# Performance work log

Hardware: AMD Instinct MI355X
Metric: run time of the kernel (lower is better)

## Reference

```python
import jax, jax.numpy as jnp
import numpy as np

D_MODEL = 768; N_HEADS = 24; HEAD_DIM = 64; D_INNER = 1536
D_STATE = 128; CONV_K = 4
CONV_DIM = D_INNER + 2 * D_STATE              # 1792
PROJ_DIM = 2 * D_INNER + 2 * D_STATE + N_HEADS  # 3352
CHUNK = 256; N_LAYERS = 24; EPS = 1e-5


def rms(h, w):
    return h * jax.lax.rsqrt(jnp.mean(h * h, -1, keepdims=True) + EPS) * w


def bnorm(x, g, b, m, v):
    shp = (1, -1) + (1,) * (x.ndim - 2)
    return (x - m.reshape(shp)) * (g.reshape(shp) / jnp.sqrt(v.reshape(shp) + EPS)) + b.reshape(shp)


def conv1d(x, w, b, stride, pad, groups=1):
    y = jax.lax.conv_general_dilated(x, w, (stride,), [pad], feature_group_count=groups,
                                     dimension_numbers=('NCH', 'OIH', 'NCH'))
    return y + b[None, :, None]


def ssd(X, dA, Bm, Cm, chunk):
    # X:(b,l,h,p) already multiplied by dt; dA:(b,l,h)=dt*A (negative); Bm,Cm:(b,l,h,n)
    b, l, h, p = X.shape
    n = Bm.shape[-1]
    c = l // chunk
    Xc = X.reshape(b, c, chunk, h, p)
    Bc = Bm.reshape(b, c, chunk, h, n)
    Cc = Cm.reshape(b, c, chunk, h, n)
    Ac = dA.reshape(b, c, chunk, h).transpose(0, 3, 1, 2)   # (b,h,c,k)
    Acs = jnp.cumsum(Ac, axis=-1)
    seg = Acs[..., :, None] - Acs[..., None, :]              # (b,h,c,k,k)
    tri = jnp.tril(jnp.ones((chunk, chunk), bool))
    Lm = jnp.where(tri, jnp.exp(seg), 0.0)
    Y_diag = jnp.einsum('bckhn,bcshn,bhcks,bcshp->bckhp', Cc, Bc, Lm, Xc)
    decay_states = jnp.exp(Acs[..., -1:] - Acs)              # (b,h,c,k)
    states = jnp.einsum('bckhn,bhck,bckhp->bchpn', Bc, decay_states, Xc)
    chunk_decay = jnp.exp(Acs[..., -1])                      # (b,h,c)
    def step(carry, inp):
        st, dec = inp
        return carry * dec[..., None, None] + st, carry
    _, prev = jax.lax.scan(step, jnp.zeros_like(states[:, 0]),
                           (states.transpose(1, 0, 2, 3, 4), chunk_decay.transpose(2, 0, 1)))
    prev = prev.transpose(1, 0, 2, 3, 4)                     # (b,c,h,p,n)
    Y_off = jnp.einsum('bckhn,bchpn,bhck->bckhp', Cc, prev, jnp.exp(Acs))
    return (Y_diag + Y_off).reshape(b, l, h, p)


def forward(x, c1_w, c1_b, bn1_g, bn1_b, bn1_m, bn1_v, c2_w, c2_b, bn2_g, bn2_b, bn2_m, bn2_v,
            c3_w, c3_b, bn3_g, bn3_b, bn3_m, bn3_v, ln_w, in_proj_w, conv_w, conv_b, dt_bias,
            A_log, D_skip, gn_w, out_proj_w, normf_w, fc1_w, fc1_b, bnc_g, bnc_b, bnc_m, bnc_v,
            fc2_w, fc2_b):
    gelu = lambda t: jax.nn.gelu(t, approximate=False)
    h = bnorm(gelu(conv1d(x, c1_w, c1_b, 2, (2, 2))), bn1_g, bn1_b, bn1_m, bn1_v)
    h = bnorm(gelu(conv1d(h, c2_w, c2_b, 2, (1, 1))), bn2_g, bn2_b, bn2_m, bn2_v)
    h = bnorm(gelu(conv1d(h, c3_w, c3_b, 1, (1, 1))), bn3_g, bn3_b, bn3_m, bn3_v)
    h = h.transpose(0, 2, 1)  # (B, L, D)

    def layer(h, p):
        lnw, inw, cw, cb, dtb, alog, dsk, gnw, outw = p
        b, l, _ = h.shape
        zxbcdt = rms(h, lnw) @ inw                  # (B,L,3352)
        z = zxbcdt[..., :D_INNER]
        xBC = zxbcdt[..., D_INNER:D_INNER + CONV_DIM]
        dt = jax.nn.softplus(zxbcdt[..., D_INNER + CONV_DIM:] + dtb)  # (B,L,H)
        xBC = jax.nn.silu(conv1d(xBC.transpose(0, 2, 1), cw[:, None, :], cb, 1,
                                 (CONV_K - 1, 0), groups=CONV_DIM)).transpose(0, 2, 1)
        Xh = xBC[..., :D_INNER].reshape(b, l, N_HEADS, HEAD_DIM)
        Bh = jnp.broadcast_to(xBC[..., D_INNER:D_INNER + D_STATE][:, :, None, :],
                              (b, l, N_HEADS, D_STATE))
        Ch = jnp.broadcast_to(xBC[..., D_INNER + D_STATE:][:, :, None, :],
                              (b, l, N_HEADS, D_STATE))
        dA = dt * (-jnp.exp(alog))[None, None, :]
        Y = ssd(Xh * dt[..., None], dA, Bh, Ch, CHUNK) + dsk[None, None, :, None] * Xh
        y = rms(Y.reshape(b, l, D_INNER) * jax.nn.silu(z), gnw)  # gated RMSNorm
        return h + y @ outw, None

    h, _ = jax.lax.scan(jax.checkpoint(layer), h,
                        (ln_w, in_proj_w, conv_w, conv_b, dt_bias, A_log, D_skip, gn_w, out_proj_w))
    pooled = rms(h, normf_w).mean(1)
    f = jax.nn.relu(bnorm(pooled @ fc1_w + fc1_b, bnc_g, bnc_b, bnc_m, bnc_v))
    return f @ fc2_w + fc2_b


def setup_inputs() -> dict:
    key = jax.random.key(0)
    it = iter(jax.random.split(key, 40))
    nx = lambda shp, s: jax.random.normal(next(it), shp, jnp.float32) * s
    B, L0 = 2, 4096
    inp = {}
    inp['x'] = nx((B, 12, L0), 1.0)
    inp['c1_w'] = nx((192, 12, 5), 0.1); inp['c1_b'] = jnp.zeros(192)
    inp['bn1_g'] = jnp.ones(192); inp['bn1_b'] = jnp.zeros(192)
    inp['bn1_m'] = jnp.zeros(192); inp['bn1_v'] = jnp.ones(192)
    inp['c2_w'] = nx((384, 192, 3), 0.05); inp['c2_b'] = jnp.zeros(384)
    inp['bn2_g'] = jnp.ones(384); inp['bn2_b'] = jnp.zeros(384)
    inp['bn2_m'] = jnp.zeros(384); inp['bn2_v'] = jnp.ones(384)
    inp['c3_w'] = nx((768, 384, 3), 0.05); inp['c3_b'] = jnp.zeros(768)
    inp['bn3_g'] = jnp.ones(768); inp['bn3_b'] = jnp.zeros(768)
    inp['bn3_m'] = jnp.zeros(768); inp['bn3_v'] = jnp.ones(768)
    inp['ln_w'] = jnp.ones((N_LAYERS, D_MODEL))
    inp['in_proj_w'] = nx((N_LAYERS, D_MODEL, PROJ_DIM), 0.02)
    inp['conv_w'] = nx((N_LAYERS, CONV_DIM, CONV_K), 0.2)
    inp['conv_b'] = jnp.zeros((N_LAYERS, CONV_DIM))
    inp['dt_bias'] = nx((N_LAYERS, N_HEADS), 0.5)
    inp['A_log'] = jnp.log(jnp.tile(jnp.arange(1, N_HEADS + 1, dtype=jnp.float32)[None], (N_LAYERS, 1)))
    inp['D_skip'] = jnp.ones((N_LAYERS, N_HEADS))
    inp['gn_w'] = jnp.ones((N_LAYERS, D_INNER))
    inp['out_proj_w'] = nx((N_LAYERS, D_INNER, D_MODEL), 0.02)
    inp['normf_w'] = jnp.ones(D_MODEL)
    inp['fc1_w'] = nx((D_MODEL, 512), 0.05); inp['fc1_b'] = jnp.zeros(512)
    inp['bnc_g'] = jnp.ones(512); inp['bnc_b'] = jnp.zeros(512)
    inp['bnc_m'] = jnp.zeros(512); inp['bnc_v'] = jnp.ones(512)
    inp['fc2_w'] = nx((512, 27), 0.05); inp['fc2_b'] = jnp.zeros(27)
    return inp


def reference(x, c1_w, c1_b, bn1_g, bn1_b, bn1_m, bn1_v, c2_w, c2_b, bn2_g, bn2_b, bn2_m, bn2_v,
              c3_w, c3_b, bn3_g, bn3_b, bn3_m, bn3_v, ln_w, in_proj_w, conv_w, conv_b, dt_bias,
              A_log, D_skip, gn_w, out_proj_w, normf_w, fc1_w, fc1_b, bnc_g, bnc_b, bnc_m, bnc_v,
              fc2_w, fc2_b):
    return forward(x, c1_w, c1_b, bn1_g, bn1_b, bn1_m, bn1_v, c2_w, c2_b, bn2_g, bn2_b, bn2_m,
                   bn2_v, c3_w, c3_b, bn3_g, bn3_b, bn3_m, bn3_v, ln_w, in_proj_w, conv_w,
                   conv_b, dt_bias, A_log, D_skip, gn_w, out_proj_w, normf_w, fc1_w, fc1_b,
                   bnc_g, bnc_b, bnc_m, bnc_v, fc2_w, fc2_b)
```

## Files before the change

kernel.cpp:

```cpp
#include <hip/hip_runtime.h>
#include <math.h>

#define DEV __device__ __forceinline__

constexpr int BATCH = 2;
constexpr int L0 = 4096;
constexpr int LS1 = 2048;
constexpr int LS2 = 1024;
constexpr int SEQ = 1024;
constexpr int DM = 768;
constexpr int NH = 24;
constexpr int HD = 64;
constexpr int DI = 1536;
constexpr int DSTATE = 128;
constexpr int CDIM = 1792;
constexpr int PDIM = 3352;
constexpr int PPAD = 3456;
constexpr int CHUNKC = 256;
constexpr int NCH = 4;
constexpr int NLAYER = 24;
constexpr float EPSF = 1e-5f;

constexpr int XT2_ROWS = 2050;
constexpr size_t XT2_BSTRIDE = (size_t)XT2_ROWS*192;
constexpr int XT3_ROWS = 1026;
constexpr size_t XT3_BSTRIDE = (size_t)XT3_ROWS*384;

typedef short bf16x8 __attribute__((ext_vector_type(8)));
typedef float f32x4 __attribute__((ext_vector_type(4)));

DEV float sigmoidf_(float x){ return 1.f/(1.f+expf(-x)); }
DEV float siluf_(float x){ return x*sigmoidf_(x); }
DEV float geluf_(float x){ return 0.5f*x*(1.f+erff(x*0.70710678118654752440f)); }
DEV float softplusf_(float x){ return fmaxf(x,0.f) + log1pf(expf(-fabsf(x))); }

DEV unsigned short f2bf(float x){
  union { float f; unsigned int u; } v; v.f = x;
  unsigned int u = v.u;
  unsigned int r = (u + 0x7fffu + ((u>>16)&1u)) >> 16;
  return (unsigned short)r;
}
DEV float bf2f(unsigned short u){
  union { unsigned int u; float f; } v; v.u = ((unsigned int)u)<<16; return v.f;
}

DEV void load_lds16(const void* g, void* l){
  __builtin_amdgcn_global_load_lds(
      (const __attribute__((address_space(1))) unsigned int*)g,
      (__attribute__((address_space(3))) unsigned int*)l,
      16, 0, 0);
}

DEV float block_sum_256(float v, float* red4){
  #pragma unroll
  for (int o=32;o>0;o>>=1) v += __shfl_down(v,o,64);
  int tid = threadIdx.x;
  __syncthreads();
  if ((tid&63)==0) red4[tid>>6]=v;
  __syncthreads();
  return red4[0]+red4[1]+red4[2]+red4[3];
}

__global__ __launch_bounds__(256) void conv_stem1(const float* __restrict__ x,
    const float* __restrict__ w, const float* __restrict__ bias,
    const float* __restrict__ g, const float* __restrict__ bb,
    const float* __restrict__ mn, const float* __restrict__ vr,
    float* __restrict__ out){
  int idx = blockIdx.x*256+threadIdx.x;
  if (idx >= BATCH*192*LS1) return;
  int lo = idx & (LS1-1);
  int co = (idx >> 11) % 192;
  int b  = idx / (192*LS1);
  float s = bias[co];
  const float* wr = w + co*60;
  #pragma unroll
  for (int ci=0; ci<12; ci++){
    const float* xr = x + ((size_t)(b*12+ci))*L0;
    #pragma unroll
    for (int k=0;k<5;k++){
      int li = lo*2 + k - 2;
      if (li>=0 && li<L0) s += wr[ci*5+k]*xr[li];
    }
  }
  s = geluf_(s);
  s = (s-mn[co])*(g[co]*rsqrtf(vr[co]+EPSF)) + bb[co];
  out[idx] = s;
}

__global__ __launch_bounds__(256) void wt_reorder(const float* __restrict__ w,
    unsigned short* __restrict__ o, int CO, int CI, int KK){
  int idx = blockIdx.x*256+threadIdx.x;
  if (idx >= CO*CI*KK) return;
  int ci = idx % CI;
  int k  = (idx/CI) % KK;
  int co = idx/(CI*KK);
  o[idx] = f2bf(w[(size_t)co*CI*KK + (size_t)ci*KK + k]);
}

__global__ __launch_bounds__(256) void transpose_pad_bf(const float* __restrict__ in,
    unsigned short* __restrict__ out, int R, int C,
    size_t in_bstride, size_t out_bstride){
  const float* ib = in + (size_t)blockIdx.z*in_bstride;
  unsigned short* ob = out + (size_t)blockIdx.z*out_bstride;
  __shared__ float t[32][33];
  int c0 = blockIdx.x*32, r0 = blockIdx.y*32;
  int tx = threadIdx.x & 31, ty = threadIdx.x >> 5;
  #pragma unroll
  for (int i=0;i<32;i+=8)
    t[ty+i][tx] = ib[(size_t)(r0+ty+i)*C + c0+tx];
  __syncthreads();
  #pragma unroll
  for (int i=0;i<32;i+=8)
    ob[(size_t)(c0+ty+i+1)*R + r0+tx] = f2bf(t[tx][ty+i]);
  if (blockIdx.x==0 && ty==0){
    ob[r0+tx] = 0;
    ob[(size_t)(C+1)*R + r0+tx] = 0;
  }
}

__global__ __launch_bounds__(256) void zero_rows3(unsigned short* __restrict__ xT3){
  int i = blockIdx.x*256+threadIdx.x;
  if (i >= 2*2*384) return;
  int ci = i % 384;
  int r  = (i/384) & 1;
  int b2 = i / 768;
  xT3[(size_t)b2*XT3_BSTRIDE + (size_t)(r?1025:0)*384 + ci] = 0;
}

template<int MODE>
__global__ __launch_bounds__(256,2) void gemm_stem(const unsigned short* __restrict__ A,
    const unsigned short* __restrict__ Bt,
    const float* __restrict__ bias, const float* __restrict__ g,
    const float* __restrict__ bbn, const float* __restrict__ mn,
    const float* __restrict__ vr,
    unsigned short* __restrict__ Ob, float* __restrict__ Of,
    int K, int rowStride, size_t batchStride){
  __shared__ alignas(16) unsigned short As[2][128*32];
  __shared__ alignas(16) unsigned short Bs[2][128*32];
  int tid = threadIdx.x;
  int wave = tid >> 6, lane = tid & 63;
  int mBase = blockIdx.y*128, nBase = blockIdx.x*128;
  int bidx = mBase >> 10;
  int mloc = mBase & 1023;
  const unsigned short* Ab = A + (size_t)bidx*batchStride + (size_t)mloc*rowStride;
  const size_t rs2 = (size_t)rowStride*2;
  const size_t K2 = (size_t)K*2;
  int o0 = wave*1024 + lane*16;
  int o1 = o0 + 4096;
  const char* Ag0 = (const char*)Ab + (size_t)(o0>>6)*rs2 + (o0&63);
  const char* Ag1 = (const char*)Ab + (size_t)(o1>>6)*rs2 + (o1&63);
  const char* Bg0 = (const char*)Bt + (size_t)(nBase + (o0>>6))*K2 + (o0&63);
  const char* Bg1 = (const char*)Bt + (size_t)(nBase + (o1>>6))*K2 + (o1&63);

  int wm = (wave>>1)*64, wn = (wave&1)*64;
  int ln = lane & 15, quad = lane >> 4;

  f32x4 acc[4][4];
  #pragma unroll
  for (int i=0;i<4;i++)
    #pragma unroll
    for (int j=0;j<4;j++) acc[i][j] = (f32x4){0.f,0.f,0.f,0.f};

  auto stage = [&](int buf, int k0){
    size_t kb = (size_t)k0*2;
    char* AsW = (char*)(&As[buf][0]) + wave*1024;
    char* BsW = (char*)(&Bs[buf][0]) + wave*1024;
    load_lds16(Ag0 + kb, AsW);
    load_lds16(Ag1 + kb, AsW + 4096);
    load_lds16(Bg0 + kb, BsW);
    load_lds16(Bg1 + kb, BsW + 4096);
  };

  stage(0, 0);
  int cur = 0;
  for (int k0=0; k0<K; k0+=32){
    __syncthreads();
    if (k0+32 < K) stage(cur^1, k0+32);
    bf16x8 a[4], b[4];
    #pragma unroll
    for (int mt=0;mt<4;mt++)
      a[mt] = *(const bf16x8*)((const char*)(&As[cur][0]) + (size_t)(wm+mt*16+ln)*64 + quad*16);
    #pragma unroll
    for (int nt=0;nt<4;nt++)
      b[nt] = *(const bf16x8*)((const char*)(&Bs[cur][0]) + (size_t)(wn+nt*16+ln)*64 + quad*16);
    #pragma unroll
    for (int mt=0;mt<4;mt++)
      #pragma unroll
      for (int nt=0;nt<4;nt++)
        acc[mt][nt] = __builtin_amdgcn_mfma_f32_16x16x32_bf16(a[mt], b[nt], acc[mt][nt], 0,0,0);
    cur ^= 1;
  }

  #pragma unroll
  for (int nt=0;nt<4;nt++){
    int col = nBase + wn + nt*16 + ln;
    float bs = bias[col];
    float sc = g[col]*rsqrtf(vr[col]+EPSF);
    float bnm2 = mn[col], bnb2 = bbn[col];
    #pragma unroll
    for (int mt=0;mt<4;mt++){
      int row0 = mBase + wm + mt*16 + quad*4;
      #pragma unroll
      for (int r=0;r<4;r++){
        int row = row0 + r;
        float v = acc[mt][nt][r] + bs;
        v = geluf_(v);
        v = (v-bnm2)*sc + bnb2;
        if (MODE==0){
          int b2 = row >> 10, lr = row & 1023;
          Ob[(size_t)b2*XT3_BSTRIDE + (size_t)(lr+1)*384 + col] = f2bf(v);
        } else {
          Of[(size_t)row*DM + col] = v;
        }
      }
    }
  }
}

template<int BF>
__global__ __launch_bounds__(256) void rmsnorm768(const float* __restrict__ in,
    const float* __restrict__ w, float* __restrict__ outf, unsigned short* __restrict__ outb){
  int row = blockIdx.x;
  const float* p = in + (size_t)row*DM;
  float v0[3]; float ss=0.f;
  #pragma unroll
  for (int t=0;t<3;t++){ float q = p[threadIdx.x + t*256]; v0[t]=q; ss+=q*q; }
  __shared__ float red[4];
  float tot = block_sum_256(ss, red);
  float sc = rsqrtf(tot*(1.f/DM) + EPSF);
  #pragma unroll
  for (int t=0;t<3;t++){
    int d = threadIdx.x + t*256;
    float o = v0[t]*sc*w[d];
    if (BF) outb[(size_t)row*DM + d] = f2bf(o);
    else    outf[(size_t)row*DM + d] = o;
  }
}

__global__ __launch_bounds__(256) void transpose_cvt_l(const float* __restrict__ in0,
    unsigned short* __restrict__ out0, int R, int Cin, int Cpad,
    size_t in_lstride, size_t out_lstride,
    const float* __restrict__ rsc, size_t rsc_stride){
  const float* in = in0 + (size_t)blockIdx.z*in_lstride;
  unsigned short* out = out0 + (size_t)blockIdx.z*out_lstride;
  const float* rs = rsc ? (rsc + (size_t)blockIdx.z*rsc_stride) : nullptr;
  __shared__ float t[32][33];
  int c0 = blockIdx.x*32, r0 = blockIdx.y*32;
  int tx = threadIdx.x & 31, ty = threadIdx.x >> 5;
  #pragma unroll
  for (int i=0;i<32;i+=8){
    int r = r0+ty+i, c = c0+tx;
    float v = (c<Cin) ? in[(size_t)r*Cin + c] : 0.f;
    if (rs) v *= rs[r];
    t[ty+i][tx] = v;
  }
  __syncthreads();
  #pragma unroll
  for (int i=0;i<32;i+=8){
    int c = c0+ty+i, r = r0+tx;
    if (c < Cpad) out[(size_t)c*R + r] = f2bf(t[tx][ty+i]);
  }
}

template<int MODE>
__global__ __launch_bounds__(256,2) void gemm_bf16(const unsigned short* __restrict__ A,
    const unsigned short* __restrict__ Bt, float* __restrict__ Cf,
    unsigned short* __restrict__ Cb, int Ntrue, int K, int ldc){
  __shared__ alignas(16) unsigned short As[2][128*32];
  __shared__ alignas(16) unsigned short Bs[2][128*32];
  int tid = threadIdx.x;
  int wave = tid >> 6, lane = tid & 63;
  int mBase = blockIdx.y*128, nBase = blockIdx.x*128;
  const size_t K2 = (size_t)K*2;
  int o0 = wave*1024 + lane*16;
  int o1 = o0 + 4096;
  const char* Ag0 = (const char*)A + (size_t)(mBase + (o0>>6))*K2 + (o0&63);
  const char* Ag1 = (const char*)A + (size_t)(mBase + (o1>>6))*K2 + (o1&63);
  const char* Bg0 = (const char*)Bt + (size_t)(nBase + (o0>>6))*K2 + (o0&63);
  const char* Bg1 = (const char*)Bt + (size_t)(nBase + (o1>>6))*K2 + (o1&63);

  int wm = (wave>>1)*64, wn = (wave&1)*64;
  int ln = lane & 15, quad = lane >> 4;

  f32x4 acc[4][4];
  #pragma unroll
  for (int i=0;i<4;i++)
    #pragma unroll
    for (int j=0;j<4;j++) acc[i][j] = (f32x4){0.f,0.f,0.f,0.f};

  auto stage = [&](int buf, int k0){
    size_t kb = (size_t)k0*2;
    char* AsW = (char*)(&As[buf][0]) + wave*1024;
    char* BsW = (char*)(&Bs[buf][0]) + wave*1024;
    load_lds16(Ag0 + kb, AsW);
    load_lds16(Ag1 + kb, AsW + 4096);
    load_lds16(Bg0 + kb, BsW);
    load_lds16(Bg1 + kb, BsW + 4096);
  };

  stage(0, 0);
  int cur = 0;
  for (int k0=0; k0<K; k0+=32){
    __syncthreads();
    if (k0+32 < K) stage(cur^1, k0+32);
    bf16x8 a[4], b[4];
    #pragma unroll
    for (int mt=0;mt<4;mt++)
      a[mt] = *(const bf16x8*)((const char*)(&As[cur][0]) + (size_t)(wm+mt*16+ln)*64 + quad*16);
    #pragma unroll
    for (int nt=0;nt<4;nt++)
      b[nt] = *(const bf16x8*)((const char*)(&Bs[cur][0]) + (size_t)(wn+nt*16+ln)*64 + quad*16);
    #pragma unroll
    for (int mt=0;mt<4;mt++)
      #pragma unroll
      for (int nt=0;nt<4;nt++)
        acc[mt][nt] = __builtin_amdgcn_mfma_f32_16x16x32_bf16(a[mt], b[nt], acc[mt][nt], 0,0,0);
    cur ^= 1;
  }

  #pragma unroll
  for (int mt=0;mt<4;mt++){
    #pragma unroll
    for (int nt=0;nt<4;nt++){
      int col = nBase + wn + nt*16 + ln;
      int row0 = mBase + wm + mt*16 + quad*4;
      if (col < Ntrue){
        #pragma unroll
        for (int r=0;r<4;r++){
          float v = acc[mt][nt][r];
          if (MODE==2) Cb[(size_t)(row0+r)*ldc + col] = f2bf(v);
          else         Cf[(size_t)(row0+r)*ldc + col] = v;
        }
      }
    }
  }
}

__global__ __launch_bounds__(256,2) void gemm_out(const unsigned short* __restrict__ A,
    const unsigned short* __restrict__ Bt, const float* __restrict__ ssum,
    float* __restrict__ C, int N, int K){
  __shared__ alignas(16) unsigned short As[2][64*136];
  __shared__ alignas(16) unsigned short Bs[2][64*136];
  int tid = threadIdx.x;
  int wave = tid>>6, lane = tid&63, ln = lane&15, quad = lane>>4;
  int mBase = blockIdx.y*64, nBase = blockIdx.x*64;
  int srow = tid>>2, sseg = tid&3;
  const unsigned short* Ag = A + (size_t)(mBase+srow)*K;
  const unsigned short* Bg = Bt + (size_t)(nBase+srow)*K;

  bf16x8 rA[4], rB[4];
  auto ldregs = [&](int k0){
    #pragma unroll
    for (int s=0;s<4;s++){
      rA[s] = *(const bf16x8*)(Ag + k0 + (sseg+s*4)*8);
      rB[s] = *(const bf16x8*)(Bg + k0 + (sseg+s*4)*8);
    }
  };
  auto stlds = [&](int buf){
    #pragma unroll
    for (int s=0;s<4;s++){
      *(bf16x8*)&As[buf][srow*136 + (sseg+s*4)*8] = rA[s];
      *(bf16x8*)&Bs[buf][srow*136 + (sseg+s*4)*8] = rB[s];
    }
  };

  f32x4 acc[4];
  #pragma unroll
  for (int nt=0;nt<4;nt++) acc[nt] = (f32x4){0.f,0.f,0.f,0.f};

  ldregs(0); stlds(0);
  int cur = 0;
  for (int k0=0; k0<K; k0+=128){
    __syncthreads();
    bool pf = (k0+128 < K);
    if (pf) ldregs(k0+128);
    bf16x8 a[4];
    #pragma unroll
    for (int kq=0;kq<4;kq++)
      a[kq] = *(const bf16x8*)&As[cur][(wave*16+ln)*136 + kq*32 + quad*8];
    #pragma unroll
    for (int nt=0;nt<4;nt++){
      #pragma unroll
      for (int kq=0;kq<4;kq++){
        bf16x8 b = *(const bf16x8*)&Bs[cur][(nt*16+ln)*136 + kq*32 + quad*8];
        acc[nt] = __builtin_amdgcn_mfma_f32_16x16x32_bf16(a[kq], b, acc[nt], 0,0,0);
      }
    }
    if (pf) stlds(cur^1);
    cur ^= 1;
  }
  int row0 = mBase + wave*16 + quad*4;
  #pragma unroll
  for (int r=0;r<4;r++){
    int row = row0 + r;
    float rsv = rsqrtf(ssum[row]*(1.f/DI) + EPSF);
    #pragma unroll
    for (int nt=0;nt<4;nt++){
      int col = nBase + nt*16 + ln;
      float* p = C + (size_t)row*N + col;
      *p += acc[nt][r]*rsv;
    }
  }
}

__global__ __launch_bounds__(256) void dwconv8(const unsigned short* __restrict__ zxb,
    const float* __restrict__ w, const float* __restrict__ bias,
    unsigned short* __restrict__ out, float* __restrict__ ssum){
  int idx = blockIdx.x*256+threadIdx.x;
  if (idx < BATCH*SEQ) ssum[idx] = 0.f;
  if (idx >= BATCH*SEQ*(CDIM/8)) return;
  int c8 = idx % (CDIM/8);
  int l  = (idx/(CDIM/8)) % SEQ;
  int b  = idx / ((CDIM/8)*SEQ);
  int c = c8*8;
  float acc[8];
  #pragma unroll
  for (int j=0;j<8;j++) acc[j] = bias[c+j];
  const unsigned short* colbase = zxb + (size_t)(b*SEQ)*PDIM + DI + c;
  #pragma unroll
  for (int k=0;k<4;k++){
    int li = l-3+k;
    if (li>=0){
      bf16x8 v = *(const bf16x8*)(colbase + (size_t)li*PDIM);
      #pragma unroll
      for (int j=0;j<8;j++) acc[j] += w[(c+j)*4+k]*bf2f((unsigned short)v[j]);
    }
  }
  unsigned short o[8];
  #pragma unroll
  for (int j=0;j<8;j++) o[j] = f2bf(siluf_(acc[j]));
  *(bf16x8*)(out + (size_t)idx*8) = *(bf16x8*)&o[0];
}

__global__ __launch_bounds__(256) void prep_fused(const unsigned short* __restrict__ zxb,
    const unsigned short* __restrict__ xbcb,
    const float* __restrict__ dtb, const float* __restrict__ alog,
    float* __restrict__ acs, unsigned short* __restrict__ XdT,
    unsigned short* __restrict__ Xdec, unsigned short* __restrict__ BTg){
  int blk = blockIdx.x;
  int tid = threadIdx.x;
  __shared__ alignas(16) unsigned short Xs[64*72];
  __shared__ float dts[256];
  __shared__ float dec[256];
  __shared__ float wsum[4];
  if (blk < 192){
    int c = blk % NCH, h = (blk/NCH) % NH, b = blk/(NCH*NH);
    int bh = b*NH + h;
    int l = c*CHUNKC + tid;
    int lane = tid & 63, wv = tid >> 6;
    float negA = -expf(alog[h]);
    float lg = bf2f(zxb[((size_t)(b*SEQ+l))*PDIM + (DI+CDIM) + h]) + dtb[h];
    float dt = softplusf_(lg);
    dts[tid] = dt;
    float s = dt*negA;
    #pragma unroll
    for (int off=1; off<64; off<<=1){
      float t = __shfl_up(s, off, 64);
      if (lane >= off) s += t;
    }
    if (lane == 63) wsum[wv] = s;
    __syncthreads();
    float pre = 0.f, tot = 0.f;
    #pragma unroll
    for (int w=0; w<4; w++){
      float wv2 = wsum[w];
      if (w < wv) pre += wv2;
      tot += wv2;
    }
    s += pre;
    acs[(size_t)bh*SEQ + l] = s;
    dec[tid] = expf(tot - s);
    int srow = tid>>2, sseg = tid&3;
    int p = tid>>2, lq = tid&3;
    for (int lt2=0; lt2<4; lt2++){
      int lt = c*4 + lt2;
      __syncthreads();
      const unsigned short* src = xbcb + ((size_t)(b*SEQ) + lt*64 + srow)*CDIM + h*HD;
      #pragma unroll
      for (int s2=0;s2<2;s2++)
        *(bf16x8*)&Xs[srow*72 + (sseg+s2*4)*8] = *(const bf16x8*)(src + (sseg+s2*4)*8);
      __syncthreads();
      unsigned short o1[16], o2[16];
      #pragma unroll
      for (int li=0; li<16; li++){
        int j = lq*16+li;
        int lc = lt2*64 + j;
        float vv = bf2f(Xs[j*72 + p]) * dts[lc];
        o1[li] = f2bf(vv);
        o2[li] = f2bf(vv*dec[lc]);
      }
      size_t rowo = ((size_t)bh*HD + p)*SEQ + lt*64 + lq*16;
      *(bf16x8*)(XdT + rowo)     = *(bf16x8*)&o1[0];
      *(bf16x8*)(XdT + rowo + 8) = *(bf16x8*)&o1[8];
      *(bf16x8*)(Xdec + rowo)     = *(bf16x8*)&o2[0];
      *(bf16x8*)(Xdec + rowo + 8) = *(bf16x8*)&o2[8];
    }
  } else {
    int r = blk - 192;
    int nh = r & 1, lt = (r>>1) & 15, b = r >> 5;
    int srow = tid>>2, sseg = tid&3;
    const unsigned short* src = xbcb + ((size_t)(b*SEQ) + lt*64 + srow)*CDIM + DI + nh*64;
    #pragma unroll
    for (int s2=0;s2<2;s2++)
      *(bf16x8*)&Xs[srow*72 + (sseg+s2*4)*8] = *(const bf16x8*)(src + (sseg+s2*4)*8);
    __syncthreads();
    int n = tid>>2, lq = tid&3;
    unsigned short o[16];
    #pragma unroll
    for (int li=0; li<16; li++) o[li] = Xs[(lq*16+li)*72 + n];
    size_t rowo = ((size_t)b*DSTATE + nh*64 + n)*SEQ + lt*64 + lq*16;
    *(bf16x8*)(BTg + rowo)     = *(bf16x8*)&o[0];
    *(bf16x8*)(BTg + rowo + 8) = *(bf16x8*)&o[8];
  }
}

__global__ __launch_bounds__(256) void ssd_states2(const unsigned short* __restrict__ Xdec,
    const unsigned short* __restrict__ BTg, float* __restrict__ states){
  int blk = blockIdx.x;
  int nh = blk & 1;
  int r = blk >> 1;
  int h = r % NH;  r /= NH;
  int c = r % NCH;
  int b = r / NCH;
  int tid = threadIdx.x, wave = tid>>6, lane = tid&63, ln = lane&15, quad = lane>>4;
  __shared__ alignas(16) unsigned short As[64*264];
  __shared__ alignas(16) unsigned short Bs[64*264];
  int bh = b*NH + h;
  {
    int srow = tid>>2, sseg = tid&3;
    const unsigned short* ga = Xdec + ((size_t)bh*HD + srow)*SEQ + c*CHUNKC;
    const unsigned short* gb = BTg + ((size_t)b*DSTATE + nh*64 + srow)*SEQ + c*CHUNKC;
    #pragma unroll
    for (int s=0;s<8;s++){
      *(bf16x8*)&As[srow*264 + (sseg+s*4)*8] = *(const bf16x8*)(ga + (sseg+s*4)*8);
      *(bf16x8*)&Bs[srow*264 + (sseg+s*4)*8] = *(const bf16x8*)(gb + (sseg+s*4)*8);
    }
  }
  __syncthreads();
  f32x4 acc[4];
  #pragma unroll
  for (int nt=0;nt<4;nt++) acc[nt] = (f32x4){0.f,0.f,0.f,0.f};
  bf16x8 a[8];
  #pragma unroll
  for (int kq=0;kq<8;kq++)
    a[kq] = *(const bf16x8*)&As[(wave*16+ln)*264 + kq*32 + quad*8];
  #pragma unroll
  for (int nt=0;nt<4;nt++){
    #pragma unroll
    for (int kq=0;kq<8;kq++){
      bf16x8 bb = *(const bf16x8*)&Bs[(nt*16+ln)*264 + kq*32 + quad*8];
      acc[nt] = __builtin_amdgcn_mfma_f32_16x16x32_bf16(a[kq], bb, acc[nt], 0,0,0);
    }
  }
  float* sp = states + (((size_t)(b*NCH+c)*NH + h) << 13) + nh*64;
  #pragma unroll
  for (int nt=0;nt<4;nt++){
    #pragma unroll
    for (int r2=0;r2<4;r2++)
      sp[(size_t)(wave*16 + quad*4 + r2)*DSTATE + nt*16 + ln] = acc[nt][r2];
  }
}

__global__ __launch_bounds__(256) void ssd_scan(const float* __restrict__ states,
    const float* __restrict__ acs, unsigned short* __restrict__ prev){
  int idx = blockIdx.x*256+threadIdx.x;
  if (idx >= BATCH*NH*HD*DSTATE) return;
  int pn = idx & 8191;
  int bh = idx >> 13;
  int h = bh % NH, b = bh / NH;
  float carry = 0.f;
  #pragma unroll
  for (int c=0;c<NCH;c++){
    size_t o = (((size_t)(b*NCH+c)*NH + h) << 13) + pn;
    prev[o] = f2bf(carry);
    float dec = expf(acs[(b*NH+h)*SEQ + c*CHUNKC + CHUNKC-1]);
    carry = carry*dec + states[o];
  }
}

constexpr int CW_S  = 136;
constexpr int SB_S  = 72;
constexpr int XT_S  = 72;

__global__ __launch_bounds__(256,2) void ssd_diag2(
    const unsigned short* __restrict__ xbcb, const unsigned short* __restrict__ XdT,
    const float* __restrict__ acs, const unsigned short* __restrict__ prev,
    const float* __restrict__ dskip, const unsigned short* __restrict__ zxb,
    float* __restrict__ ssum, unsigned short* __restrict__ Y){
  int blk = blockIdx.x;
  int t = blk & 3;
  int r0 = blk >> 2;
  int h = r0 % NH;  r0 /= NH;
  int c = r0 % NCH;
  int b = r0 / NCH;

  int tid = threadIdx.x;
  int wave = tid>>6, lane = tid&63, ln = lane&15, quad = lane>>4;

  __shared__ float ac[CHUNKC];
  __shared__ alignas(16) unsigned short Cw[64*CW_S];
  __shared__ alignas(16) unsigned short Pv[64*CW_S];
  __shared__ alignas(16) unsigned short Bt[64*CW_S];
  __shared__ alignas(16) unsigned short Xt[64*XT_S];
  __shared__ alignas(16) unsigned short Sb[4][16*SB_S];

  const int bh = b*NH + h;
  const size_t rowbase = (size_t)(b*SEQ + c*CHUNKC);

  ac[tid] = acs[(size_t)bh*SEQ + c*CHUNKC + tid];

  {
    int srow = tid>>2, sseg = tid&3;
    const unsigned short* gc = xbcb + (rowbase + t*64 + srow)*CDIM + DI + DSTATE;
    const unsigned short* gp = prev + (((size_t)(b*NCH+c)*NH + h) << 13) + (size_t)srow*DSTATE;
    #pragma unroll
    for (int s=0;s<4;s++){
      *(bf16x8*)&Cw[srow*CW_S + (sseg+s*4)*8] = *(const bf16x8*)(gc + (sseg+s*4)*8);
      *(bf16x8*)&Pv[srow*CW_S + (sseg+s*4)*8] = *(const bf16x8*)(gp + (sseg+s*4)*8);
    }
  }
  __syncthreads();

  bf16x8 aC[4];
  #pragma unroll
  for (int kq=0;kq<4;kq++)
    aC[kq] = *(const bf16x8*)&Cw[(wave*16+ln)*CW_S + kq*32 + quad*8];

  f32x4 yacc[4];
  #pragma unroll
  for (int ps=0;ps<4;ps++) yacc[ps] = (f32x4){0.f,0.f,0.f,0.f};

  for (int jt=0; jt<=t; jt++){
    __syncthreads();
    {
      int srow = tid>>2, sseg = tid&3;
      const unsigned short* gbm = xbcb + (rowbase + jt*64 + srow)*CDIM + DI;
      #pragma unroll
      for (int s=0;s<4;s++)
        *(bf16x8*)&Bt[srow*CW_S + (sseg+s*4)*8] = *(const bf16x8*)(gbm + (sseg+s*4)*8);
      const unsigned short* gx = XdT + ((size_t)bh*HD + srow)*SEQ + c*CHUNKC + jt*64;
      #pragma unroll
      for (int s=0;s<2;s++)
        *(bf16x8*)&Xt[srow*XT_S + (sseg+s*4)*8] = *(const bf16x8*)(gx + (sseg+s*4)*8);
    }
    __syncthreads();

    #pragma unroll
    for (int js=0; js<4; js++){
      f32x4 s = (f32x4){0.f,0.f,0.f,0.f};
      #pragma unroll
      for (int kq=0;kq<4;kq++){
        bf16x8 bB = *(const bf16x8*)&Bt[(js*16+ln)*CW_S + kq*32 + quad*8];
        s = __builtin_amdgcn_mfma_f32_16x16x32_bf16(aC[kq], bB, s, 0,0,0);
      }
      int jc = jt*64 + js*16 + ln;
      #pragma unroll
      for (int r=0;r<4;r++){
        int icl = t*64 + wave*16 + quad*4 + r;
        float d = (jc<=icl) ? (ac[icl]-ac[jc]) : -1e30f;
        Sb[wave][(quad*4+r)*SB_S + js*16 + ln] = f2bf(expf(d)*s[r]);
      }
    }
    bf16x8 aS[2];
    #pragma unroll
    for (int kq=0;kq<2;kq++)
      aS[kq] = *(const bf16x8*)&Sb[wave][ln*SB_S + kq*32 + quad*8];
    #pragma unroll
    for (int ps=0;ps<4;ps++){
      #pragma unroll
      for (int kq=0;kq<2;kq++){
        bf16x8 bX = *(const bf16x8*)&Xt[(ps*16+ln)*XT_S + kq*32 + quad*8];
        yacc[ps] = __builtin_amdgcn_mfma_f32_16x16x32_bf16(aS[kq], bX, yacc[ps], 0,0,0);
      }
    }
  }

  f32x4 oacc[4];
  #pragma unroll
  for (int ps=0;ps<4;ps++) oacc[ps] = (f32x4){0.f,0.f,0.f,0.f};
  #pragma unroll
  for (int ps=0;ps<4;ps++){
    #pragma unroll
    for (int kq=0;kq<4;kq++){
      bf16x8 bP = *(const bf16x8*)&Pv[(ps*16+ln)*CW_S + kq*32 + quad*8];
      oacc[ps] = __builtin_amdgcn_mfma_f32_16x16x32_bf16(aC[kq], bP, oacc[ps], 0,0,0);
    }
  }

  float dsk = dskip[h];
  #pragma unroll
  for (int r=0;r<4;r++){
    int icl = t*64 + wave*16 + quad*4 + r;
    float ei = expf(ac[icl]);
    size_t l = rowbase + icl;
    float rss = 0.f;
    #pragma unroll
    for (int ps=0;ps<4;ps++){
      int p = ps*16 + ln;
      float xraw = bf2f(xbcb[l*CDIM + h*HD + p]);
      float zv = bf2f(zxb[l*PDIM + h*HD + p]);
      float yg = (yacc[ps][r] + ei*oacc[ps][r] + dsk*xraw) * siluf_(zv);
      Y[l*DI + h*HD + p] = f2bf(yg);
      rss += yg*yg;
    }
    rss += __shfl_down(rss, 8, 64);
    rss += __shfl_down(rss, 4, 64);
    rss += __shfl_down(rss, 2, 64);
    rss += __shfl_down(rss, 1, 64);
    if (ln == 0) atomicAdd(&ssum[l], rss);
  }
}

__global__ __launch_bounds__(256) void mean_pool(const float* __restrict__ hn,
    float* __restrict__ pooled){
  int idx = blockIdx.x*256+threadIdx.x;
  if (idx >= BATCH*DM) return;
  int b = idx / DM, d = idx % DM;
  float s = 0.f;
  for (int l=0;l<SEQ;l++) s += hn[((size_t)(b*SEQ+l))*DM + d];
  pooled[idx] = s * (1.f/SEQ);
}

__global__ __launch_bounds__(512) void head_k(const float* __restrict__ pooled,
    const float* __restrict__ w1, const float* __restrict__ b1,
    const float* __restrict__ g, const float* __restrict__ bb,
    const float* __restrict__ mn, const float* __restrict__ vr,
    const float* __restrict__ w2, const float* __restrict__ b2,
    float* __restrict__ out){
  int b = blockIdx.x;
  int j = threadIdx.x;
  __shared__ float f[512];
  __shared__ float pl[DM];
  for (int t=j; t<DM; t+=512) pl[t] = pooled[b*DM+t];
  __syncthreads();
  float s = b1[j];
  for (int k=0;k<DM;k++) s += pl[k]*w1[k*512+j];
  s = (s-mn[j])*(g[j]*rsqrtf(vr[j]+EPSF)) + bb[j];
  f[j] = fmaxf(s,0.f);
  __syncthreads();
  if (j < 27){
    float o = b2[j];
    for (int k=0;k<512;k++) o += f[k]*w2[k*27+j];
    out[b*27+j] = o;
  }
}

extern "C" void kernel_launch(void* const* d_in, const int* in_sizes, int n_in,
                              void* d_out, int out_size, void* d_ws, size_t ws_size,
                              hipStream_t stream){
  const float* x      = (const float*)d_in[0];
  const float* c1_w   = (const float*)d_in[1];
  const float* c1_b   = (const float*)d_in[2];
  const float* bn1_g  = (const float*)d_in[3];
  const float* bn1_b  = (const float*)d_in[4];
  const float* bn1_m  = (const float*)d_in[5];
  const float* bn1_v  = (const float*)d_in[6];
  const float* c2_w   = (const float*)d_in[7];
  const float* c2_b   = (const float*)d_in[8];
  const float* bn2_g  = (const float*)d_in[9];
  const float* bn2_b  = (const float*)d_in[10];
  const float* bn2_m  = (const float*)d_in[11];
  const float* bn2_v  = (const float*)d_in[12];
  const float* c3_w   = (const float*)d_in[13];
  const float* c3_b   = (const float*)d_in[14];
  const float* bn3_g  = (const float*)d_in[15];
  const float* bn3_b  = (const float*)d_in[16];
  const float* bn3_m  = (const float*)d_in[17];
  const float* bn3_v  = (const float*)d_in[18];
  const float* ln_w   = (const float*)d_in[19];
  const float* inpw   = (const float*)d_in[20];
  const float* convw  = (const float*)d_in[21];
  const float* convb  = (const float*)d_in[22];
  const float* dtb    = (const float*)d_in[23];
  const float* alog   = (const float*)d_in[24];
  const float* dskip  = (const float*)d_in[25];
  const float* gnw    = (const float*)d_in[26];
  const float* outw   = (const float*)d_in[27];
  const float* normfw = (const float*)d_in[28];
  const float* fc1w   = (const float*)d_in[29];
  const float* fc1b   = (const float*)d_in[30];
  const float* bncg   = (const float*)d_in[31];
  const float* bncb   = (const float*)d_in[32];
  const float* bncm   = (const float*)d_in[33];
  const float* bncv   = (const float*)d_in[34];
  const float* fc2w   = (const float*)d_in[35];
  const float* fc2b   = (const float*)d_in[36];
  (void)in_sizes; (void)n_in; (void)out_size;

  char* ws = (char*)d_ws;
  size_t off = 0;
  auto alloc = [&](size_t bytes){
    char* p = ws + off;
    off += (bytes + 255) & ~(size_t)255;
    return (void*)p;
  };
  float* h1  = (float*)alloc((size_t)BATCH*192*LS1*4);
  float* h   = (float*)alloc((size_t)BATCH*SEQ*DM*4);
  float* hn  = (float*)alloc((size_t)BATCH*SEQ*DM*4);
  unsigned short* zxb = (unsigned short*)alloc((size_t)BATCH*SEQ*PDIM*2);
  unsigned short* xbcb= (unsigned short*)alloc((size_t)BATCH*SEQ*CDIM*2);
  float* acs = (float*)alloc((size_t)BATCH*NH*SEQ*4);
  float* st  = (float*)alloc((size_t)BATCH*NCH*NH*HD*DSTATE*4);
  unsigned short* pv  = (unsigned short*)alloc((size_t)BATCH*NCH*NH*HD*DSTATE*2);
  unsigned short* Y   = (unsigned short*)alloc((size_t)BATCH*SEQ*DI*2);
  float* pooled = (float*)alloc((size_t)BATCH*DM*4);
  unsigned short* hnb   = (unsigned short*)alloc((size_t)BATCH*SEQ*DM*2);
  float* ssum = (float*)alloc((size_t)BATCH*SEQ*4);
  unsigned short* XdTg  = (unsigned short*)alloc((size_t)BATCH*NH*HD*SEQ*2);
  unsigned short* Xdecg = (unsigned short*)alloc((size_t)BATCH*NH*HD*SEQ*2);
  unsigned short* BTg   = (unsigned short*)alloc((size_t)BATCH*DSTATE*SEQ*2);
  unsigned short* xT2   = (unsigned short*)alloc((size_t)BATCH*XT2_BSTRIDE*2);
  unsigned short* xT3   = (unsigned short*)alloc((size_t)BATCH*XT3_BSTRIDE*2);
  unsigned short* wt2   = (unsigned short*)alloc((size_t)384*576*2);
  unsigned short* wt3   = (unsigned short*)alloc((size_t)768*1152*2);

  const size_t wtin_l  = (size_t)PPAD*DM;
  const size_t wtout_l = (size_t)DM*DI;
  size_t base_off = off;
  size_t big_bytes = (wtin_l + wtout_l)*NLAYER*2 + 512;
  bool big = (ws_size >= base_off + big_bytes);
  unsigned short *wtinA, *wtoutA;
  if (big){
    wtinA  = (unsigned short*)alloc(wtin_l*NLAYER*2);
    wtoutA = (unsigned short*)alloc(wtout_l*NLAYER*2);
  } else {
    wtinA  = (unsigned short*)alloc(wtin_l*2);
    wtoutA = (unsigned short*)alloc(wtout_l*2);
  }

  wt_reorder<<<(384*192*3+255)/256,256,0,stream>>>(c2_w, wt2, 384, 192, 3);
  wt_reorder<<<(768*384*3+255)/256,256,0,stream>>>(c3_w, wt3, 768, 384, 3);
  zero_rows3<<<(2*2*384+255)/256,256,0,stream>>>(xT3);
  if (big){
    transpose_cvt_l<<<dim3(PPAD/32, DM/32, NLAYER),256,0,stream>>>(
        inpw, wtinA, DM, PDIM, PPAD, (size_t)DM*PDIM, wtin_l, nullptr, 0);
    transpose_cvt_l<<<dim3(DM/32, DI/32, NLAYER),256,0,stream>>>(
        outw, wtoutA, DI, DM, DM, (size_t)DI*DM, wtout_l, gnw, (size_t)DI);
  }

  conv_stem1<<<(BATCH*192*LS1+255)/256,256,0,stream>>>(x, c1_w,c1_b, bn1_g,bn1_b,bn1_m,bn1_v, h1);
  transpose_pad_bf<<<dim3(LS1/32, 192/32, BATCH),256,0,stream>>>(
      h1, xT2, 192, LS1, (size_t)192*LS1, XT2_BSTRIDE);
  gemm_stem<0><<<dim3(384/128, 16),256,0,stream>>>(
      xT2, wt2, c2_b, bn2_g, bn2_b, bn2_m, bn2_v, xT3, nullptr,
      576, 384, XT2_BSTRIDE);
  gemm_stem<1><<<dim3(768/128, 16),256,0,stream>>>(
      xT3, wt3, c3_b, bn3_g, bn3_b, bn3_m, bn3_v, nullptr, h,
      1152, 384, XT3_BSTRIDE);

  const int M = BATCH*SEQ;
  for (int l=0; l<NLAYER; l++){
    unsigned short* wtin  = big ? (wtinA  + (size_t)l*wtin_l)  : wtinA;
    unsigned short* wtout = big ? (wtoutA + (size_t)l*wtout_l) : wtoutA;
    if (!big){
      transpose_cvt_l<<<dim3(PPAD/32, DM/32, 1),256,0,stream>>>(
          inpw + (size_t)l*DM*PDIM, wtin, DM, PDIM, PPAD, 0, 0, nullptr, 0);
      transpose_cvt_l<<<dim3(DM/32, DI/32, 1),256,0,stream>>>(
          outw + (size_t)l*DI*DM, wtout, DI, DM, DM, 0, 0, gnw + (size_t)l*DI, 0);
    }

    rmsnorm768<1><<<M,256,0,stream>>>(h, ln_w + (size_t)l*DM, nullptr, hnb);
    gemm_bf16<2><<<dim3(PPAD/128, M/128),256,0,stream>>>(hnb, wtin, nullptr, zxb, PDIM, DM, PDIM);
    dwconv8<<<(BATCH*SEQ*(CDIM/8)+255)/256,256,0,stream>>>(zxb, convw + (size_t)l*CDIM*4, convb + (size_t)l*CDIM, xbcb, ssum);
    prep_fused<<<256,256,0,stream>>>(zxb, xbcb, dtb + l*NH, alog + l*NH, acs, XdTg, Xdecg, BTg);
    ssd_states2<<<BATCH*NCH*NH*2,256,0,stream>>>(Xdecg, BTg, st);
    ssd_scan<<<(BATCH*NH*HD*DSTATE+255)/256,256,0,stream>>>(st, acs, pv);
    ssd_diag2<<<BATCH*NCH*NH*4,256,0,stream>>>(xbcb, XdTg, acs, pv, dskip + l*NH, zxb, ssum, Y);
    gemm_out<<<dim3(DM/64, M/64),256,0,stream>>>(Y, wtout, ssum, h, DM, DI);
  }

  rmsnorm768<0><<<M,256,0,stream>>>(h, normfw, hn, nullptr);
  mean_pool<<<(BATCH*DM+255)/256,256,0,stream>>>(hn, pooled);
  head_k<<<BATCH,512,0,stream>>>(pooled, fc1w, fc1b, bncg,bncb,bncm,bncv, fc2w, fc2b, (float*)d_out);
}
```

Baseline: 3.755 ms.

## Fuse depthwise conv into prep kernel and widen GEMM K-tile to 64

The separate dwconv8 kernel is removed. The causal depthwise conv plus SiLU is now computed inside prep_fused, which writes xbcb and also feeds the transposed X and B tiles straight from registers and LDS, and the grid grows to cover the C channels. Separately, both bf16 GEMMs switch from a K-step of 32 to 64, doubling LDS per block and halving the number of barriers per K-loop. The fusion saves a launch and a round trip of the conv output, but neighbouring rows' conv inputs are recomputed across blocks. The larger LDS footprint may reduce occupancy.

```diff
diff --git a/kernel.cpp b/kernel.cpp
--- a/kernel.cpp
+++ b/kernel.cpp
@@ -135,8 +135,8 @@
     const float* __restrict__ vr,
     unsigned short* __restrict__ Ob, float* __restrict__ Of,
     int K, int rowStride, size_t batchStride){
-  __shared__ alignas(16) unsigned short As[2][128*32];
-  __shared__ alignas(16) unsigned short Bs[2][128*32];
+  __shared__ alignas(16) unsigned short As[2][128*64];
+  __shared__ alignas(16) unsigned short Bs[2][128*64];
   int tid = threadIdx.x;
   int wave = tid >> 6, lane = tid & 63;
   int mBase = blockIdx.y*128, nBase = blockIdx.x*128;
@@ -145,12 +145,13 @@
   const unsigned short* Ab = A + (size_t)bidx*batchStride + (size_t)mloc*rowStride;
   const size_t rs2 = (size_t)rowStride*2;
   const size_t K2 = (size_t)K*2;
-  int o0 = wave*1024 + lane*16;
-  int o1 = o0 + 4096;
-  const char* Ag0 = (const char*)Ab + (size_t)(o0>>6)*rs2 + (o0&63);
-  const char* Ag1 = (const char*)Ab + (size_t)(o1>>6)*rs2 + (o1&63);
-  const char* Bg0 = (const char*)Bt + (size_t)(nBase + (o0>>6))*K2 + (o0&63);
-  const char* Bg1 = (const char*)Bt + (size_t)(nBase + (o1>>6))*K2 + (o1&63);
+  const char* Ag[4]; const char* Bg[4];
+  #pragma unroll
+  for (int c2=0;c2<4;c2++){
+    int o = c2*4096 + wave*1024 + lane*16;
+    Ag[c2] = (const char*)Ab + (size_t)(o>>7)*rs2 + (o&127);
+    Bg[c2] = (const char*)Bt + (size_t)(nBase + (o>>7))*K2 + (o&127);
+  }
 
   int wm = (wave>>1)*64, wn = (wave&1)*64;
   int ln = lane & 15, quad = lane >> 4;
@@ -163,31 +164,35 @@
 
   auto stage = [&](int buf, int k0){
     size_t kb = (size_t)k0*2;
-    char* AsW = (char*)(&As[buf][0]) + wave*1024;
-    char* BsW = (char*)(&Bs[buf][0]) + wave*1024;
-    load_lds16(Ag0 + kb, AsW);
-    load_lds16(Ag1 + kb, AsW + 4096);
-    load_lds16(Bg0 + kb, BsW);
-    load_lds16(Bg1 + kb, BsW + 4096);
+    #pragma unroll
+    for (int c2=0;c2<4;c2++){
+      load_lds16(Ag[c2] + kb, (char*)(&As[buf][0]) + c2*4096 + wave*1024);
+      load_lds16(Bg[c2] + kb, (char*)(&Bs[buf][0]) + c2*4096 + wave*1024);
+    }
   };
 
   stage(0, 0);
   int cur = 0;
-  for (int k0=0; k0<K; k0+=32){
+  for (int k0=0; k0<K; k0+=64){
     __syncthreads();
-    if (k0+32 < K) stage(cur^1, k0+32);
-    bf16x8 a[4], b[4];
-    #pragma unroll
-    for (int mt=0;mt<4;mt++)
-      a[mt] = *(const bf16x8*)((const char*)(&As[cur][0]) + (size_t)(wm+mt*16+ln)*64 + quad*16);
-    #pragma unroll
-    for (int nt=0;nt<4;nt++)
-      b[nt] = *(const bf16x8*)((const char*)(&Bs[cur][0]) + (size_t)(wn+nt*16+ln)*64 + quad*16);
-    #pragma unroll
-    for (int mt=0;mt<4;mt++)
+    if (k0+64 < K) stage(cur^1, k0+64);
+    bf16x8 a[2][4], b[2][4];
+    #pragma unroll
+    for (int kh=0;kh<2;kh++){
+      #pragma unroll
+      for (int mt=0;mt<4;mt++)
+        a[kh][mt] = *(const bf16x8*)((const char*)(&As[cur][0]) + (size_t)(wm+mt*16+ln)*128 + kh*64 + quad*16);
       #pragma unroll
       for (int nt=0;nt<4;nt++)
-        acc[mt][nt] = __builtin_amdgcn_mfma_f32_16x16x32_bf16(a[mt], b[nt], acc[mt][nt], 0,0,0);
+        b[kh][nt] = *(const bf16x8*)((const char*)(&Bs[cur][0]) + (size_t)(wn+nt*16+ln)*128 + kh*64 + quad*16);
+    }
+    #pragma unroll
+    for (int kh=0;kh<2;kh++)
+      #pragma unroll
+      for (int mt=0;mt<4;mt++)
+        #pragma unroll
+        for (int nt=0;nt<4;nt++)
+          acc[mt][nt] = __builtin_amdgcn_mfma_f32_16x16x32_bf16(a[kh][mt], b[kh][nt], acc[mt][nt], 0,0,0);
     cur ^= 1;
   }
 
@@ -266,18 +271,19 @@
 __global__ __launch_bounds__(256,2) void gemm_bf16(const unsigned short* __restrict__ A,
     const unsigned short* __restrict__ Bt, float* __restrict__ Cf,
     unsigned short* __restrict__ Cb, int Ntrue, int K, int ldc){
-  __shared__ alignas(16) unsigned short As[2][128*32];
-  __shared__ alignas(16) unsigned short Bs[2][128*32];
+  __shared__ alignas(16) unsigned short As[2][128*64];
+  __shared__ alignas(16) unsigned short Bs[2][128*64];
   int tid = threadIdx.x;
   int wave = tid >> 6, lane = tid & 63;
   int mBase = blockIdx.y*128, nBase = blockIdx.x*128;
   const size_t K2 = (size_t)K*2;
-  int o0 = wave*1024 + lane*16;
-  int o1 = o0 + 4096;
-  const char* Ag0 = (const char*)A + (size_t)(mBase + (o0>>6))*K2 + (o0&63);
-  const char* Ag1 = (const char*)A + (size_t)(mBase + (o1>>6))*K2 + (o1&63);
-  const char* Bg0 = (const char*)Bt + (size_t)(nBase + (o0>>6))*K2 + (o0&63);
-  const char* Bg1 = (const char*)Bt + (size_t)(nBase + (o1>>6))*K2 + (o1&63);
+  const char* Ag[4]; const char* Bg[4];
+  #pragma unroll
+  for (int c2=0;c2<4;c2++){
+    int o = c2*4096 + wave*1024 + lane*16;
+    Ag[c2] = (const char*)A + (size_t)(mBase + (o>>7))*K2 + (o&127);
+    Bg[c2] = (const char*)Bt + (size_t)(nBase + (o>>7))*K2 + (o&127);
+  }
 
   int wm = (wave>>1)*64, wn = (wave&1)*64;
   int ln = lane & 15, quad = lane >> 4;
@@ -290,31 +296,35 @@
 
   auto stage = [&](int buf, int k0){
     size_t kb = (size_t)k0*2;
-    char* AsW = (char*)(&As[buf][0]) + wave*1024;
-    char* BsW = (char*)(&Bs[buf][0]) + wave*1024;
-    load_lds16(Ag0 + kb, AsW);
-    load_lds16(Ag1 + kb, AsW + 4096);
-    load_lds16(Bg0 + kb, BsW);
-    load_lds16(Bg1 + kb, BsW + 4096);
+    #pragma unroll
+    for (int c2=0;c2<4;c2++){
+      load_lds16(Ag[c2] + kb, (char*)(&As[buf][0]) + c2*4096 + wave*1024);
+      load_lds16(Bg[c2] + kb, (char*)(&Bs[buf][0]) + c2*4096 + wave*1024);
+    }
   };
 
   stage(0, 0);
   int cur = 0;
-  for (int k0=0; k0<K; k0+=32){
+  for (int k0=0; k0<K; k0+=64){
     __syncthreads();
-    if (k0+32 < K) stage(cur^1, k0+32);
-    bf16x8 a[4], b[4];
-    #pragma unroll
-    for (int mt=0;mt<4;mt++)
-      a[mt] = *(const bf16x8*)((const char*)(&As[cur][0]) + (size_t)(wm+mt*16+ln)*64 + quad*16);
-    #pragma unroll
-    for (int nt=0;nt<4;nt++)
-      b[nt] = *(const bf16x8*)((const char*)(&Bs[cur][0]) + (size_t)(wn+nt*16+ln)*64 + quad*16);
-    #pragma unroll
-    for (int mt=0;mt<4;mt++)
+    if (k0+64 < K) stage(cur^1, k0+64);
+    bf16x8 a[2][4], b[2][4];
+    #pragma unroll
+    for (int kh=0;kh<2;kh++){
+      #pragma unroll
+      for (int mt=0;mt<4;mt++)
+        a[kh][mt] = *(const bf16x8*)((const char*)(&As[cur][0]) + (size_t)(wm+mt*16+ln)*128 + kh*64 + quad*16);
       #pragma unroll
       for (int nt=0;nt<4;nt++)
-        acc[mt][nt] = __builtin_amdgcn_mfma_f32_16x16x32_bf16(a[mt], b[nt], acc[mt][nt], 0,0,0);
+        b[kh][nt] = *(const bf16x8*)((const char*)(&Bs[cur][0]) + (size_t)(wn+nt*16+ln)*128 + kh*64 + quad*16);
+    }
+    #pragma unroll
+    for (int kh=0;kh<2;kh++)
+      #pragma unroll
+      for (int mt=0;mt<4;mt++)
+        #pragma unroll
+        for (int nt=0;nt<4;nt++)
+          acc[mt][nt] = __builtin_amdgcn_mfma_f32_16x16x32_bf16(a[kh][mt], b[kh][nt], acc[mt][nt], 0,0,0);
     cur ^= 1;
   }
 
@@ -403,53 +413,32 @@
   }
 }
 
-__global__ __launch_bounds__(256) void dwconv8(const unsigned short* __restrict__ zxb,
-    const float* __restrict__ w, const float* __restrict__ bias,
-    unsigned short* __restrict__ out, float* __restrict__ ssum){
-  int idx = blockIdx.x*256+threadIdx.x;
-  if (idx < BATCH*SEQ) ssum[idx] = 0.f;
-  if (idx >= BATCH*SEQ*(CDIM/8)) return;
-  int c8 = idx % (CDIM/8);
-  int l  = (idx/(CDIM/8)) % SEQ;
-  int b  = idx / ((CDIM/8)*SEQ);
-  int c = c8*8;
-  float acc[8];
-  #pragma unroll
-  for (int j=0;j<8;j++) acc[j] = bias[c+j];
-  const unsigned short* colbase = zxb + (size_t)(b*SEQ)*PDIM + DI + c;
-  #pragma unroll
-  for (int k=0;k<4;k++){
-    int li = l-3+k;
-    if (li>=0){
-      bf16x8 v = *(const bf16x8*)(colbase + (size_t)li*PDIM);
-      #pragma unroll
-      for (int j=0;j<8;j++) acc[j] += w[(c+j)*4+k]*bf2f((unsigned short)v[j]);
-    }
-  }
-  unsigned short o[8];
-  #pragma unroll
-  for (int j=0;j<8;j++) o[j] = f2bf(siluf_(acc[j]));
-  *(bf16x8*)(out + (size_t)idx*8) = *(bf16x8*)&o[0];
-}
-
 __global__ __launch_bounds__(256) void prep_fused(const unsigned short* __restrict__ zxb,
-    const unsigned short* __restrict__ xbcb,
+    unsigned short* __restrict__ xbcb,
+    const float* __restrict__ cw, const float* __restrict__ cb,
     const float* __restrict__ dtb, const float* __restrict__ alog,
     float* __restrict__ acs, unsigned short* __restrict__ XdT,
-    unsigned short* __restrict__ Xdec, unsigned short* __restrict__ BTg){
+    unsigned short* __restrict__ Xdec, unsigned short* __restrict__ BTg,
+    float* __restrict__ ssum){
   int blk = blockIdx.x;
   int tid = threadIdx.x;
   __shared__ alignas(16) unsigned short Xs[64*72];
   __shared__ float dts[256];
   __shared__ float dec[256];
   __shared__ float wsum[4];
+  __shared__ float wsh[256];
+  __shared__ float bsh[64];
   if (blk < 192){
     int c = blk % NCH, h = (blk/NCH) % NH, b = blk/(NCH*NH);
     int bh = b*NH + h;
-    int l = c*CHUNKC + tid;
+    int cb0 = h*64;
+    wsh[tid] = cw[(cb0 + (tid>>2))*4 + (tid&3)];
+    if (tid < 64) bsh[tid] = cb[cb0 + tid];
+    if (h == 0) ssum[(size_t)b*SEQ + c*CHUNKC + tid] = 0.f;
+    int l0 = c*CHUNKC + tid;
     int lane = tid & 63, wv = tid >> 6;
     float negA = -expf(alog[h]);
-    float lg = bf2f(zxb[((size_t)(b*SEQ+l))*PDIM + (DI+CDIM) + h]) + dtb[h];
+    float lg = bf2f(zxb[((size_t)(b*SEQ+l0))*PDIM + (DI+CDIM) + h]) + dtb[h];
     float dt = softplusf_(lg);
     dts[tid] = dt;
     float s = dt*negA;
@@ -468,17 +457,37 @@
       tot += wv2;
     }
     s += pre;
-    acs[(size_t)bh*SEQ + l] = s;
+    acs[(size_t)bh*SEQ + l0] = s;
     dec[tid] = expf(tot - s);
     int srow = tid>>2, sseg = tid&3;
     int p = tid>>2, lq = tid&3;
     for (int lt2=0; lt2<4; lt2++){
       int lt = c*4 + lt2;
       __syncthreads();
-      const unsigned short* src = xbcb + ((size_t)(b*SEQ) + lt*64 + srow)*CDIM + h*HD;
-      #pragma unroll
-      for (int s2=0;s2<2;s2++)
-        *(bf16x8*)&Xs[srow*72 + (sseg+s2*4)*8] = *(const bf16x8*)(src + (sseg+s2*4)*8);
+      {
+        int l = lt*64 + srow;
+        #pragma unroll
+        for (int s2=0;s2<2;s2++){
+          int cg = (sseg+s2*4)*8;
+          float a8[8];
+          #pragma unroll
+          for (int j=0;j<8;j++) a8[j] = bsh[cg+j];
+          #pragma unroll
+          for (int k=0;k<4;k++){
+            int li = l-3+k;
+            if (li>=0){
+              bf16x8 v = *(const bf16x8*)(zxb + ((size_t)(b*SEQ+li))*PDIM + DI + cb0 + cg);
+              #pragma unroll
+              for (int j=0;j<8;j++) a8[j] += wsh[(cg+j)*4+k]*bf2f((unsigned short)v[j]);
+            }
+          }
+          unsigned short ov[8];
+          #pragma unroll
+          for (int j=0;j<8;j++) ov[j] = f2bf(siluf_(a8[j]));
+          *(bf16x8*)&Xs[srow*72 + cg] = *(bf16x8*)&ov[0];
+          *(bf16x8*)(xbcb + ((size_t)(b*SEQ+l))*CDIM + cb0 + cg) = *(bf16x8*)&ov[0];
+        }
+      }
       __syncthreads();
       unsigned short o1[16], o2[16];
       #pragma unroll
@@ -497,20 +506,44 @@
     }
   } else {
     int r = blk - 192;
-    int nh = r & 1, lt = (r>>1) & 15, b = r >> 5;
+    int nh2 = r & 3, lt = (r>>2) & 15, b = r >> 6;
+    int cb0 = DI + nh2*64;
+    wsh[tid] = cw[(cb0 + (tid>>2))*4 + (tid&3)];
+    if (tid < 64) bsh[tid] = cb[cb0 + tid];
+    __syncthreads();
     int srow = tid>>2, sseg = tid&3;
-    const unsigned short* src = xbcb + ((size_t)(b*SEQ) + lt*64 + srow)*CDIM + DI + nh*64;
-    #pragma unroll
-    for (int s2=0;s2<2;s2++)
-      *(bf16x8*)&Xs[srow*72 + (sseg+s2*4)*8] = *(const bf16x8*)(src + (sseg+s2*4)*8);
-    __syncthreads();
-    int n = tid>>2, lq = tid&3;
-    unsigned short o[16];
-    #pragma unroll
-    for (int li=0; li<16; li++) o[li] = Xs[(lq*16+li)*72 + n];
-    size_t rowo = ((size_t)b*DSTATE + nh*64 + n)*SEQ + lt*64 + lq*16;
-    *(bf16x8*)(BTg + rowo)     = *(bf16x8*)&o[0];
-    *(bf16x8*)(BTg + rowo + 8) = *(bf16x8*)&o[8];
+    int l = lt*64 + srow;
+    #pragma unroll
+    for (int s2=0;s2<2;s2++){
+      int cg = (sseg+s2*4)*8;
+      float a8[8];
+      #pragma unroll
+      for (int j=0;j<8;j++) a8[j] = bsh[cg+j];
+      #pragma unroll
+      for (int k=0;k<4;k++){
+        int li = l-3+k;
+        if (li>=0){
+          bf16x8 v = *(const bf16x8*)(zxb + ((size_t)(b*SEQ+li))*PDIM + DI + cb0 + cg);
+          #pragma unroll
+          for (int j=0;j<8;j++) a8[j] += wsh[(cg+j)*4+k]*bf2f((unsigned short)v[j]);
+        }
+      }
+      unsigned short ov[8];
+      #pragma unroll
+      for (int j=0;j<8;j++) ov[j] = f2bf(siluf_(a8[j]));
+      *(bf16x8*)(xbcb + ((size_t)(b*SEQ+l))*CDIM + cb0 + cg) = *(bf16x8*)&ov[0];
+      if (nh2 < 2) *(bf16x8*)&Xs[srow*72 + cg] = *(bf16x8*)&ov[0];
+    }
+    if (nh2 < 2){
+      __syncthreads();
+      int n = tid>>2, lq = tid&3;
+      unsigned short o[16];
+      #pragma unroll
+      for (int li=0; li<16; li++) o[li] = Xs[(lq*16+li)*72 + n];
+      size_t rowo = ((size_t)b*DSTATE + nh2*64 + n)*SEQ + lt*64 + lq*16;
+      *(bf16x8*)(BTg + rowo)     = *(bf16x8*)&o[0];
+      *(bf16x8*)(BTg + rowo + 8) = *(bf16x8*)&o[8];
+    }
   }
 }
 
@@ -861,8 +894,8 @@
 
     rmsnorm768<1><<<M,256,0,stream>>>(h, ln_w + (size_t)l*DM, nullptr, hnb);
     gemm_bf16<2><<<dim3(PPAD/128, M/128),256,0,stream>>>(hnb, wtin, nullptr, zxb, PDIM, DM, PDIM);
-    dwconv8<<<(BATCH*SEQ*(CDIM/8)+255)/256,256,0,stream>>>(zxb, convw + (size_t)l*CDIM*4, convb + (size_t)l*CDIM, xbcb, ssum);
-    prep_fused<<<256,256,0,stream>>>(zxb, xbcb, dtb + l*NH, alog + l*NH, acs, XdTg, Xdecg, BTg);
+    prep_fused<<<320,256,0,stream>>>(zxb, xbcb, convw + (size_t)l*CDIM*4, convb + (size_t)l*CDIM,
+        dtb + l*NH, alog + l*NH, acs, XdTg, Xdecg, BTg, ssum);
     ssd_states2<<<BATCH*NCH*NH*2,256,0,stream>>>(Xdecg, BTg, st);
     ssd_scan<<<(BATCH*NH*HD*DSTATE+255)/256,256,0,stream>>>(st, acs, pv);
     ssd_diag2<<<BATCH*NCH*NH*4,256,0,stream>>>(xbcb, XdTg, acs, pv, dskip + l*NH, zxb, ssum, Y);
```

Result: faster. 3.354 ms (-10.7%).
